# Optimization experiments

Measured on AMD Instinct MI355X. Metric: run time of the kernel, lower is better.

## Reference

```python
import jax, jax.numpy as jnp
import numpy as np

B, IN, C, M = 256, 512, 4, 6
S1, S2 = 255, 63          # neurons per layer excluding the prepended bias unit
K = 2 ** M                # contexts per neuron
P = 1e-3                  # pred_clipping
LMIN = float(np.log(P / (1.0 - P)))
LMAX = -LMIN
LR = 1e-3                 # constant learning rate
WCLIP = 5.0               # weight_clipping
BASE_BIAS = 0.0           # fixed base bias logit (original draws uniform in [LMIN, LMAX])


def setup_inputs() -> dict:
    key = jax.random.key(0)
    ks = jax.random.split(key, 10)
    x = jax.random.uniform(ks[0], (B, IN), dtype=jnp.float32)
    target = jax.random.randint(ks[1], (B,), 0, C, dtype=jnp.int32)
    cmaps1 = jax.random.normal(ks[2], (C, S1, M, IN), dtype=jnp.float32)
    w1 = jax.random.uniform(ks[3], (C, S1, K, IN), dtype=jnp.float32) * (2.0 / IN)
    bias1 = jax.random.uniform(ks[4], (1, 1, C), dtype=jnp.float32, minval=LMIN, maxval=LMAX)
    cmaps2 = jax.random.normal(ks[5], (C, S2, M, IN), dtype=jnp.float32)
    w2 = jax.random.uniform(ks[6], (C, S2, K, S1 + 1), dtype=jnp.float32) * (2.0 / (S1 + 1))
    bias2 = jax.random.uniform(ks[7], (1, 1, C), dtype=jnp.float32, minval=LMIN, maxval=LMAX)
    cmaps3 = jax.random.normal(ks[8], (C, 1, M, IN), dtype=jnp.float32)
    w3 = jax.random.uniform(ks[9], (C, 1, K, S2 + 1), dtype=jnp.float32) * (2.0 / (S2 + 1))
    return {"x": x, "target": target, "cmaps1": cmaps1, "w1": w1, "bias1": bias1,
            "cmaps2": cmaps2, "w2": w2, "bias2": bias2, "cmaps3": cmaps3, "w3": w3}


def _layer(logit3, context, tgt, cmaps, weights, bias):
    # logit3: (B, I, Cin) with Cin in {1, C}; context: (B, IN); tgt: (B, C) one-hot
    # cmaps: (C, S, M, IN); weights: (C, S, K, I)
    Cn, S = weights.shape[0], weights.shape[1]
    Bn = context.shape[0]
    # context halfspace gating -> per-(class, neuron, sample) context index
    dist = jnp.einsum('csmk,bk->csmb', cmaps, context)          # (C,S,M,B)
    conv = (2 ** jnp.arange(M, dtype=jnp.int32)).reshape(1, 1, M, 1)
    idx = jnp.sum((dist > 0.0).astype(jnp.int32) * conv, axis=2)  # (C,S,B)
    ci = jnp.arange(Cn)[:, None, None]
    si = jnp.arange(S)[None, :, None]
    sel = weights[ci, si, idx]                                  # gather: (C,S,B,I)
    lg = jnp.broadcast_to(logit3, (Bn, logit3.shape[1], Cn))    # (B,I,C)
    out = jnp.clip(jnp.einsum('csbi,bic->csb', sel, lg), LMIN, LMAX)
    out_t = jnp.transpose(out, (2, 1, 0))                       # (B,S,C)
    # online gradient-style update scattered back into the weight table
    diff = jax.nn.sigmoid(out_t) - tgt[:, None, :]              # (B,S,C)
    upd = LR * diff[..., None] * jnp.transpose(lg, (0, 2, 1))[:, None, :, :]  # (B,S,C,I)
    new_w = weights.at[ci, si, idx].set(
        jnp.clip(sel - jnp.transpose(upd, (2, 1, 0, 3)), -WCLIP, WCLIP))
    if bias is not None:
        out_t = jnp.concatenate([jnp.broadcast_to(bias, (Bn, 1, Cn)), out_t], axis=1)
    return out_t, new_w


def reference(x, target, cmaps1, w1, bias1, cmaps2, w2, bias2, cmaps3, w3):
    tgt = jax.nn.one_hot(target, C, dtype=x.dtype)              # (B,C)
    xb = jnp.clip(x, P, 1.0 - P)
    l0 = jnp.log(xb / (1.0 - xb)).at[:, 0].set(BASE_BIAS)       # base predictions in logit space
    out1, nw1 = _layer(l0[:, :, None], x, tgt, cmaps1, w1, bias1)  # (B,256,C)
    out2, nw2 = _layer(out1, x, tgt, cmaps2, w2, bias2)            # (B,64,C)
    out3, nw3 = _layer(out2, x, tgt, cmaps3, w3, None)             # (B,1,C)
    logits = out3[:, 0, :]                                         # (B,C)
    return (logits, nw1, nw2, nw3)
```

## Files before the change

kernel.cpp:

```cpp
#include <hip/hip_runtime.h>
#include <math.h>

#define B_   256
#define IN_  512
#define C_   4
#define M_   6
#define K_   64
#define S1_  255
#define S2_  63

#define NBLK1 (C_ * S1_)
#define NBLK2 (C_ * S2_)
#define NBLK3 (C_)
#define NBLK_ALL (NBLK1 + NBLK2 + NBLK3)

#define LMIN_ (-6.906754778648554f)
#define LMAX_ ( 6.906754778648554f)
#define LR_   0.001f
#define WCLIP_ 5.0f

typedef float v4f __attribute__((ext_vector_type(4)));

__device__ __forceinline__ float clampf(float v, float lo, float hi) {
    return fminf(fmaxf(v, lo), hi);
}

__global__ __launch_bounds__(256) void prep_kernel(const float* __restrict__ x,
                                                   const float* __restrict__ bias1,
                                                   const float* __restrict__ bias2,
                                                   float* __restrict__ xT,
                                                   float* __restrict__ l0,
                                                   float* __restrict__ l0T,
                                                   float* __restrict__ out1T,
                                                   float* __restrict__ out1RM,
                                                   float* __restrict__ out2T,
                                                   float* __restrict__ out2RM) {
    __shared__ float tx_[32][33];
    __shared__ float tl_[32][33];
    const int i0 = (blockIdx.x & 15) * 32;
    const int b0 = (blockIdx.x >> 4) * 32;
    const int tx = threadIdx.x & 31;
    const int ty = threadIdx.x >> 5;
#pragma unroll
    for (int r = 0; r < 4; ++r) {
        int bb = b0 + ty + 8 * r;
        int ii = i0 + tx;
        float xv = x[(size_t)bb * IN_ + ii];
        float xc = clampf(xv, 0.001f, 0.999f);
        float lv = (ii == 0) ? 0.0f : logf(xc / (1.0f - xc));
        l0[(size_t)bb * IN_ + ii] = lv;
        tx_[ty + 8 * r][tx] = xv;
        tl_[ty + 8 * r][tx] = lv;
    }
    __syncthreads();
#pragma unroll
    for (int r = 0; r < 4; ++r) {
        int ii = i0 + ty + 8 * r;
        int bb = b0 + tx;
        xT[(size_t)ii * B_ + bb]  = tx_[tx][ty + 8 * r];
        l0T[(size_t)ii * B_ + bb] = tl_[tx][ty + 8 * r];
    }
    int gid = blockIdx.x * 256 + threadIdx.x;
    if (gid < C_ * B_) {
        int c = gid >> 8, b = gid & 255;
        float b1 = bias1[c], b2 = bias2[c];
        out1T[((size_t)c * (S1_ + 1)) * B_ + b] = b1;
        out1RM[((size_t)c * B_ + b) * (S1_ + 1)] = b1;
        out2T[((size_t)c * (S2_ + 1)) * B_ + b] = b2;
        out2RM[((size_t)c * B_ + b) * (S2_ + 1)] = b2;
    }
}

__global__ __launch_bounds__(256) void route_kernel(
    const float* __restrict__ xT,
    const float* __restrict__ cmaps1,
    const float* __restrict__ cmaps2,
    const float* __restrict__ cmaps3,
    int* __restrict__ idx_buf)
{
    __shared__ float sacc[3][2][M_][B_];
    const int wv   = __builtin_amdgcn_readfirstlane(threadIdx.x >> 6);
    const int lane = threadIdx.x & 63;
    const int t0   = blockIdx.x * 2;

    const float* cmp[2];
#pragma unroll
    for (int u = 0; u < 2; ++u) {
        int bid = t0 + u;
        if (bid < NBLK1)              cmp[u] = cmaps1 + (size_t)bid * M_ * IN_;
        else if (bid < NBLK1 + NBLK2) cmp[u] = cmaps2 + (size_t)(bid - NBLK1) * M_ * IN_;
        else                          cmp[u] = cmaps3 + (size_t)(bid - NBLK1 - NBLK2) * M_ * IN_;
    }

    float acc[2][4][M_];
#pragma unroll
    for (int u = 0; u < 2; ++u)
#pragma unroll
        for (int jb = 0; jb < 4; ++jb)
#pragma unroll
            for (int m = 0; m < M_; ++m) acc[u][jb][m] = 0.0f;

    const int kw = wv * 128;
    for (int k0 = kw; k0 < kw + 128; k0 += 8) {
        float xv[8][4];
#pragma unroll
        for (int j = 0; j < 8; ++j)
#pragma unroll
            for (int jb = 0; jb < 4; ++jb)
                xv[j][jb] = xT[(size_t)(k0 + j) * B_ + 64 * jb + lane];
#pragma unroll
        for (int j = 0; j < 8; ++j)
#pragma unroll
            for (int u = 0; u < 2; ++u)
#pragma unroll
                for (int m = 0; m < M_; ++m) {
                    float cv = cmp[u][(size_t)m * IN_ + k0 + j];
#pragma unroll
                    for (int jb = 0; jb < 4; ++jb)
                        acc[u][jb][m] = fmaf(cv, xv[j][jb], acc[u][jb][m]);
                }
    }

    if (wv > 0) {
#pragma unroll
        for (int u = 0; u < 2; ++u)
#pragma unroll
            for (int jb = 0; jb < 4; ++jb)
#pragma unroll
                for (int m = 0; m < M_; ++m)
                    sacc[wv - 1][u][m][64 * jb + lane] = acc[u][jb][m];
    }
    __syncthreads();
    if (wv == 0) {
#pragma unroll
        for (int u = 0; u < 2; ++u)
#pragma unroll
            for (int jb = 0; jb < 4; ++jb) {
                int b = 64 * jb + lane;
                int myidx = 0;
#pragma unroll
                for (int m = 0; m < M_; ++m) {
                    float t = acc[u][jb][m] + sacc[0][u][m][b] + sacc[1][u][m][b] + sacc[2][u][m][b];
                    myidx |= (t > 0.0f) ? (1 << m) : 0;
                }
                idx_buf[(size_t)(t0 + u) * B_ + b] = myidx;
            }
    }
}


template<int DIN, int KSPL>
__device__ __forceinline__ void dot_body(
    int bid,
    const float* __restrict__ lgT, long lgT_sc,
    const float* __restrict__ w,
    const int* __restrict__ idx_buf,
    float* __restrict__ pdot,
    int S, float* wl)
{
    constexpr int KR  = DIN / KSPL;
    static_assert(KR == 64, "k-slice must be 64");
    constexpr int PAD = 65;

    const int tile = bid / KSPL;
    const int ks   = bid % KSPL;
    const int c    = tile / S;
    const int tid  = threadIdx.x;
    const int b    = tid;
    const int k0   = ks * KR;

    const int myrow = idx_buf[(size_t)tile * B_ + b];

    const float* wp = w + (size_t)tile * K_ * DIN + k0;
#pragma unroll
    for (int j = 0; j < 4; ++j) {
        int f   = tid + 256 * j;
        int row = f >> 4;
        int q   = (f & 15) << 2;
        float4 v = *(const float4*)(wp + (size_t)row * DIN + q);
        wl[row * PAD + q + 0] = v.x;
        wl[row * PAD + q + 1] = v.y;
        wl[row * PAD + q + 2] = v.z;
        wl[row * PAD + q + 3] = v.w;
    }
    __syncthreads();

    const float* lgp = lgT + (size_t)c * lgT_sc + (size_t)k0 * B_ + b;
    const float* wr  = wl + myrow * PAD;
    float dot = 0.0f;
    for (int kk = 0; kk < KR; kk += 8) {
        float lv[8];
#pragma unroll
        for (int t = 0; t < 8; ++t) lv[t] = lgp[(size_t)(kk + t) * B_];
#pragma unroll
        for (int t = 0; t < 8; ++t) dot = fmaf(wr[kk + t], lv[t], dot);
    }
    pdot[((size_t)tile * KSPL + ks) * B_ + b] = dot;
}

template<int DIN>
__device__ __forceinline__ void update_body(
    int ub,
    const float* __restrict__ w,
    const float* __restrict__ lgRM, long lg_sc,
    const int* __restrict__ win_g,
    const float* __restrict__ dw_g,
    float* __restrict__ nw,
    int SK)
{
    constexpr int QPR = DIN / 4;
    constexpr int QSH = (DIN == 512) ? 7 : (DIN == 256) ? 6 : 4;
    const int base = ub * 2048 + threadIdx.x;
#pragma unroll
    for (int j = 0; j < 8; ++j) {
        int Q   = base + j * 256;
        int row = Q >> QSH;
        int col = (Q & (QPR - 1)) << 2;
        float4 wv = *(const float4*)(w + (size_t)row * DIN + col);
        int bw = win_g[row];
        if (bw >= 0) {
            float d = dw_g[row];
            int cc  = row / SK;
            const float4 lv = *(const float4*)(lgRM + (size_t)cc * lg_sc + (size_t)bw * DIN + col);
            wv.x = clampf(wv.x - d * lv.x, -WCLIP_, WCLIP_);
            wv.y = clampf(wv.y - d * lv.y, -WCLIP_, WCLIP_);
            wv.z = clampf(wv.z - d * lv.z, -WCLIP_, WCLIP_);
            wv.w = clampf(wv.w - d * lv.w, -WCLIP_, WCLIP_);
        }
        v4f o = {wv.x, wv.y, wv.z, wv.w};
        __builtin_nontemporal_store(o, (v4f*)(nw + (size_t)row * DIN + col));
    }
}

template<int DIN, int KSPL>
__global__ __launch_bounds__(256) void dot_kernel(
    const float* __restrict__ lgT, long lgT_sc,
    const float* __restrict__ w,
    const int* __restrict__ idx_buf,
    float* __restrict__ pdot, int S)
{
    __shared__ float wl[K_ * 65];
    dot_body<DIN, KSPL>(blockIdx.x, lgT, lgT_sc, w, idx_buf, pdot, S, wl);
}

__global__ __launch_bounds__(256) void fin_kernel(
    const float* __restrict__ pdot, int KSPL,
    const int* __restrict__ idx_buf,
    const int* __restrict__ target,
    float* __restrict__ onextT,
    float* __restrict__ onextRM,
    int* __restrict__ win_g,
    float* __restrict__ dw_g,
    int S)
{
    __shared__ float diff_s[B_];
    __shared__ int   win_s[K_];
    const int tile = blockIdx.x;
    const int c    = tile / S;
    const int s    = tile - c * S;
    const int b    = threadIdx.x;

    if (b < K_) win_s[b] = -1;

    float dot = 0.0f;
    for (int j = 0; j < KSPL; ++j)
        dot += pdot[((size_t)tile * KSPL + j) * B_ + b];

    float outv = clampf(dot, LMIN_, LMAX_);
    onextT[((size_t)c * (S + 1) + (s + 1)) * B_ + b] = outv;
    onextRM[((size_t)c * B_ + b) * (size_t)(S + 1) + (s + 1)] = outv;

    float tg = (target[b] == c) ? 1.0f : 0.0f;
    diff_s[b] = 1.0f / (1.0f + expf(-outv)) - tg;
    const int myrow = idx_buf[(size_t)tile * B_ + b];
    __syncthreads();
    atomicMax(&win_s[myrow], b);
    __syncthreads();
    if (b < K_) {
        int bw = win_s[b];
        win_g[(size_t)tile * K_ + b] = bw;
        dw_g[(size_t)tile * K_ + b]  = (bw >= 0) ? LR_ * diff_s[bw] : 0.0f;
    }
}

template<int DIN_D, int KSPL_D, int DIN_U>
__global__ __launch_bounds__(256) void mix_kernel(
    const float* __restrict__ lgT, long lgT_sc,
    const float* __restrict__ wD,
    const int* __restrict__ idxD,
    float* __restrict__ pdot, int SD, int ndot,
    const float* __restrict__ wU,
    const float* __restrict__ lgRM, long lg_sc,
    const int* __restrict__ win_g,
    const float* __restrict__ dw_g,
    float* __restrict__ nwU, int SKU)
{
    __shared__ float wl[K_ * 65];
    if ((int)blockIdx.x < ndot)
        dot_body<DIN_D, KSPL_D>(blockIdx.x, lgT, lgT_sc, wD, idxD, pdot, SD, wl);
    else
        update_body<DIN_U>(blockIdx.x - ndot, wU, lgRM, lg_sc, win_g, dw_g, nwU, SKU);
}

__global__ __launch_bounds__(256) void fin3u_kernel(
    const float* __restrict__ pdot,
    const int* __restrict__ idx3,
    const int* __restrict__ target,
    const float* __restrict__ lgRM, long lg_sc,
    const float* __restrict__ w3,
    float* __restrict__ nw3,
    float* __restrict__ logits)
{
    __shared__ float diff_s[B_];
    __shared__ float dw_s[K_];
    __shared__ int   win_s[K_];
    const int c = blockIdx.x;
    const int b = threadIdx.x;

    if (b < K_) win_s[b] = -1;

    float outv = clampf(pdot[(size_t)c * B_ + b], LMIN_, LMAX_);
    logits[(size_t)b * C_ + c] = outv;
    float tg = (target[b] == c) ? 1.0f : 0.0f;
    diff_s[b] = 1.0f / (1.0f + expf(-outv)) - tg;
    const int myrow = idx3[(size_t)c * B_ + b];
    __syncthreads();
    atomicMax(&win_s[myrow], b);
    __syncthreads();
    if (b < K_) {
        int bw = win_s[b];
        dw_s[b] = (bw >= 0) ? LR_ * diff_s[bw] : 0.0f;
    }
    __syncthreads();

    const float* lgc = lgRM + (size_t)c * lg_sc;
    const float* wp  = w3  + (size_t)c * K_ * 64;
    float*       nwp = nw3 + (size_t)c * K_ * 64;
#pragma unroll
    for (int j = 0; j < 4; ++j) {
        int Q   = b + 256 * j;
        int row = Q >> 4;
        int col = (Q & 15) << 2;
        float4 wv = *(const float4*)(wp + row * 64 + col);
        int bw = win_s[row];
        if (bw >= 0) {
            float d = dw_s[row];
            const float4 lv = *(const float4*)(lgc + (size_t)bw * 64 + col);
            wv.x = clampf(wv.x - d * lv.x, -WCLIP_, WCLIP_);
            wv.y = clampf(wv.y - d * lv.y, -WCLIP_, WCLIP_);
            wv.z = clampf(wv.z - d * lv.z, -WCLIP_, WCLIP_);
            wv.w = clampf(wv.w - d * lv.w, -WCLIP_, WCLIP_);
        }
        v4f o = {wv.x, wv.y, wv.z, wv.w};
        __builtin_nontemporal_store(o, (v4f*)(nwp + row * 64 + col));
    }
}

extern "C" void kernel_launch(void* const* d_in, const int* in_sizes, int n_in,
                              void* d_out, int out_size, void* d_ws, size_t ws_size,
                              hipStream_t stream) {
    const float* x      = (const float*)d_in[0];
    const int*   target = (const int*)  d_in[1];
    const float* cmaps1 = (const float*)d_in[2];
    const float* w1     = (const float*)d_in[3];
    const float* bias1  = (const float*)d_in[4];
    const float* cmaps2 = (const float*)d_in[5];
    const float* w2     = (const float*)d_in[6];
    const float* bias2  = (const float*)d_in[7];
    const float* cmaps3 = (const float*)d_in[8];
    const float* w3     = (const float*)d_in[9];
    float* out = (float*)d_out;

    float* xT      = (float*)d_ws;
    float* l0      = xT     + (size_t)IN_ * B_;
    float* l0T     = l0     + (size_t)B_ * IN_;
    float* out1T   = l0T    + (size_t)IN_ * B_;
    float* out1RM  = out1T  + (size_t)C_ * (S1_ + 1) * B_;
    float* out2T   = out1RM + (size_t)C_ * B_ * (S1_ + 1);
    float* out2RM  = out2T  + (size_t)C_ * (S2_ + 1) * B_;
    float* pdot    = out2RM + (size_t)C_ * B_ * (S2_ + 1);
    float* dw_g    = pdot   + (size_t)NBLK1 * 8 * B_;
    int*   win_g   = (int*)(dw_g + (size_t)NBLK_ALL * K_);
    int*   idx_buf = (int*)(win_g + (size_t)NBLK_ALL * K_);

    float* logits = out;
    float* nw1 = out + (size_t)B_ * C_;
    float* nw2 = nw1 + (size_t)C_ * S1_ * K_ * IN_;
    float* nw3 = nw2 + (size_t)C_ * S2_ * K_ * (S1_ + 1);

    const int* idx1 = idx_buf;
    const int* idx2 = idx_buf + (size_t)NBLK1 * B_;
    const int* idx3 = idx_buf + (size_t)(NBLK1 + NBLK2) * B_;
    int*   win1 = win_g;                         float* dw1 = dw_g;
    int*   win2 = win_g + NBLK1 * K_;            float* dw2 = dw_g + NBLK1 * K_;

    prep_kernel<<<dim3(128), dim3(256), 0, stream>>>(
        x, bias1, bias2, xT, l0, l0T, out1T, out1RM, out2T, out2RM);

    route_kernel<<<dim3(NBLK_ALL / 2), dim3(256), 0, stream>>>(
        xT, cmaps1, cmaps2, cmaps3, idx_buf);

    dot_kernel<512, 8><<<dim3(NBLK1 * 8), dim3(256), 0, stream>>>(
        l0T, 0L, w1, idx1, pdot, S1_);
    fin_kernel<<<dim3(NBLK1), dim3(256), 0, stream>>>(
        pdot, 8, idx1, target, out1T, out1RM, win1, dw1, S1_);

    mix_kernel<256, 4, 512><<<dim3(NBLK2 * 4 + NBLK1 * 4), dim3(256), 0, stream>>>(
        out1T, (long)(S1_ + 1) * B_, w2, idx2, pdot, S2_, NBLK2 * 4,
        w1, l0, 0L, win1, dw1, nw1, S1_ * K_);
    fin_kernel<<<dim3(NBLK2), dim3(256), 0, stream>>>(
        pdot, 4, idx2, target, out2T, out2RM, win2, dw2, S2_);

    mix_kernel<64, 1, 256><<<dim3(NBLK3 + NBLK2 * 2), dim3(256), 0, stream>>>(
        out2T, (long)(S2_ + 1) * B_, w3, idx3, pdot, 1, NBLK3,
        w2, out1RM, (long)B_ * (S1_ + 1), win2, dw2, nw2, S2_ * K_);

    fin3u_kernel<<<dim3(NBLK3), dim3(256), 0, stream>>>(
        pdot, idx3, target, out2RM, (long)B_ * (S2_ + 1), w3, nw3, logits);
}
```

Before: 138.2 us.

## Fuse dot and finalize stages into 512-thread blocks, removing pdot round-trips

Split-K dot kernels and their separate finalize kernels are merged: each tile is now handled by one 512-thread block whose two halves each cover half of the input dimension and reduce through shared memory before doing clamp, sigmoid diff and winner selection in place. This removes the pdot global buffer, two kernel launches and the serialization between partial-dot and finalize passes. The last-layer update reuses the weights staged in LDS instead of reloading them. The trade-off is fewer, larger blocks for layer 1 (1020 instead of 8160), which lowers parallelism and gives less latency hiding while each block walks over K sequentially.

```diff
diff --git a/kernel.cpp b/kernel.cpp
--- a/kernel.cpp
+++ b/kernel.cpp
@@ -148,54 +148,77 @@
     }
 }
 
-
-template<int DIN, int KSPL>
-__device__ __forceinline__ void dot_body(
-    int bid,
+template<int DIN>
+__device__ __forceinline__ void dotfin_body(
+    int tile,
     const float* __restrict__ lgT, long lgT_sc,
     const float* __restrict__ w,
     const int* __restrict__ idx_buf,
-    float* __restrict__ pdot,
-    int S, float* wl)
-{
-    constexpr int KR  = DIN / KSPL;
-    static_assert(KR == 64, "k-slice must be 64");
-    constexpr int PAD = 65;
-
-    const int tile = bid / KSPL;
-    const int ks   = bid % KSPL;
-    const int c    = tile / S;
-    const int tid  = threadIdx.x;
-    const int b    = tid;
-    const int k0   = ks * KR;
-
+    const int* __restrict__ target,
+    float* __restrict__ onextT,
+    float* __restrict__ onextRM,
+    int* __restrict__ win_g,
+    float* __restrict__ dw_g,
+    int S,
+    float* wl, float* part_s, float* diff_s, int* win_s)
+{
+    constexpr int HALF = DIN / 2;
+    constexpr int NR   = HALF / 64;
+    const int c   = tile / S;
+    const int s   = tile - c * S;
+    const int tid = threadIdx.x;
+    const int kh  = __builtin_amdgcn_readfirstlane(tid >> 8);
+    const int b   = tid & 255;
+
+    if (tid < K_) win_s[tid] = -1;
     const int myrow = idx_buf[(size_t)tile * B_ + b];
 
-    const float* wp = w + (size_t)tile * K_ * DIN + k0;
-#pragma unroll
-    for (int j = 0; j < 4; ++j) {
-        int f   = tid + 256 * j;
-        int row = f >> 4;
-        int q   = (f & 15) << 2;
-        float4 v = *(const float4*)(wp + (size_t)row * DIN + q);
-        wl[row * PAD + q + 0] = v.x;
-        wl[row * PAD + q + 1] = v.y;
-        wl[row * PAD + q + 2] = v.z;
-        wl[row * PAD + q + 3] = v.w;
-    }
-    __syncthreads();
-
-    const float* lgp = lgT + (size_t)c * lgT_sc + (size_t)k0 * B_ + b;
-    const float* wr  = wl + myrow * PAD;
+    const float* wp  = w + (size_t)tile * K_ * DIN + kh * HALF;
+    float*       dst = wl + kh * (K_ * 65);
     float dot = 0.0f;
-    for (int kk = 0; kk < KR; kk += 8) {
-        float lv[8];
-#pragma unroll
-        for (int t = 0; t < 8; ++t) lv[t] = lgp[(size_t)(kk + t) * B_];
-#pragma unroll
-        for (int t = 0; t < 8; ++t) dot = fmaf(wr[kk + t], lv[t], dot);
-    }
-    pdot[((size_t)tile * KSPL + ks) * B_ + b] = dot;
+#pragma unroll
+    for (int r = 0; r < NR; ++r) {
+        const float* src = wp + r * 64;
+#pragma unroll
+        for (int j = 0; j < 4; ++j) {
+            int f   = b + 256 * j;
+            int row = f >> 4;
+            int q   = (f & 15) << 2;
+            float4 v = *(const float4*)(src + (size_t)row * DIN + q);
+            dst[row * 65 + q + 0] = v.x;
+            dst[row * 65 + q + 1] = v.y;
+            dst[row * 65 + q + 2] = v.z;
+            dst[row * 65 + q + 3] = v.w;
+        }
+        __syncthreads();
+        const float* lgp = lgT + (size_t)c * lgT_sc + (size_t)(kh * HALF + r * 64) * B_ + b;
+        const float* wr  = dst + myrow * 65;
+        for (int kk = 0; kk < 64; kk += 8) {
+            float lv[8];
+#pragma unroll
+            for (int t = 0; t < 8; ++t) lv[t] = lgp[(size_t)(kk + t) * B_];
+#pragma unroll
+            for (int t = 0; t < 8; ++t) dot = fmaf(wr[kk + t], lv[t], dot);
+        }
+        __syncthreads();
+    }
+    if (kh == 1) part_s[b] = dot;
+    __syncthreads();
+    if (kh == 0) {
+        float total = dot + part_s[b];
+        float outv = clampf(total, LMIN_, LMAX_);
+        onextT[((size_t)c * (S + 1) + (s + 1)) * B_ + b] = outv;
+        onextRM[((size_t)c * B_ + b) * (size_t)(S + 1) + (s + 1)] = outv;
+        float tg = (target[b] == c) ? 1.0f : 0.0f;
+        diff_s[b] = 1.0f / (1.0f + expf(-outv)) - tg;
+        atomicMax(&win_s[myrow], b);
+    }
+    __syncthreads();
+    if (tid < K_) {
+        int bw = win_s[tid];
+        win_g[(size_t)tile * K_ + tid] = bw;
+        dw_g[(size_t)tile * K_ + tid]  = (bw >= 0) ? LR_ * diff_s[bw] : 0.0f;
+    }
 }
 
 template<int DIN>
@@ -209,11 +232,11 @@
     int SK)
 {
     constexpr int QPR = DIN / 4;
-    constexpr int QSH = (DIN == 512) ? 7 : (DIN == 256) ? 6 : 4;
+    constexpr int QSH = (DIN == 512) ? 7 : 6;
     const int base = ub * 2048 + threadIdx.x;
 #pragma unroll
-    for (int j = 0; j < 8; ++j) {
-        int Q   = base + j * 256;
+    for (int j = 0; j < 4; ++j) {
+        int Q   = base + j * 512;
         int row = Q >> QSH;
         int col = (Q & (QPR - 1)) << 2;
         float4 wv = *(const float4*)(w + (size_t)row * DIN + col);
@@ -232,116 +255,109 @@
     }
 }
 
-template<int DIN, int KSPL>
-__global__ __launch_bounds__(256) void dot_kernel(
-    const float* __restrict__ lgT, long lgT_sc,
-    const float* __restrict__ w,
-    const int* __restrict__ idx_buf,
-    float* __restrict__ pdot, int S)
-{
-    __shared__ float wl[K_ * 65];
-    dot_body<DIN, KSPL>(blockIdx.x, lgT, lgT_sc, w, idx_buf, pdot, S, wl);
-}
-
-__global__ __launch_bounds__(256) void fin_kernel(
-    const float* __restrict__ pdot, int KSPL,
-    const int* __restrict__ idx_buf,
+__global__ __launch_bounds__(512) void dotfin1_kernel(
+    const float* __restrict__ l0T,
+    const float* __restrict__ w1,
+    const int* __restrict__ idx1,
     const int* __restrict__ target,
-    float* __restrict__ onextT,
-    float* __restrict__ onextRM,
-    int* __restrict__ win_g,
-    float* __restrict__ dw_g,
-    int S)
-{
+    float* __restrict__ out1T, float* __restrict__ out1RM,
+    int* __restrict__ win1, float* __restrict__ dw1)
+{
+    __shared__ float wl[2 * K_ * 65];
+    __shared__ float part_s[B_];
     __shared__ float diff_s[B_];
     __shared__ int   win_s[K_];
-    const int tile = blockIdx.x;
-    const int c    = tile / S;
-    const int s    = tile - c * S;
-    const int b    = threadIdx.x;
-
-    if (b < K_) win_s[b] = -1;
-
-    float dot = 0.0f;
-    for (int j = 0; j < KSPL; ++j)
-        dot += pdot[((size_t)tile * KSPL + j) * B_ + b];
-
-    float outv = clampf(dot, LMIN_, LMAX_);
-    onextT[((size_t)c * (S + 1) + (s + 1)) * B_ + b] = outv;
-    onextRM[((size_t)c * B_ + b) * (size_t)(S + 1) + (s + 1)] = outv;
-
-    float tg = (target[b] == c) ? 1.0f : 0.0f;
-    diff_s[b] = 1.0f / (1.0f + expf(-outv)) - tg;
-    const int myrow = idx_buf[(size_t)tile * B_ + b];
-    __syncthreads();
-    atomicMax(&win_s[myrow], b);
-    __syncthreads();
-    if (b < K_) {
-        int bw = win_s[b];
-        win_g[(size_t)tile * K_ + b] = bw;
-        dw_g[(size_t)tile * K_ + b]  = (bw >= 0) ? LR_ * diff_s[bw] : 0.0f;
-    }
-}
-
-template<int DIN_D, int KSPL_D, int DIN_U>
-__global__ __launch_bounds__(256) void mix_kernel(
+    dotfin_body<512>(blockIdx.x, l0T, 0L, w1, idx1, target,
+                     out1T, out1RM, win1, dw1, S1_, wl, part_s, diff_s, win_s);
+}
+
+__global__ __launch_bounds__(512) void mix2_kernel(
+    const float* __restrict__ out1T,
+    const float* __restrict__ w2,
+    const int* __restrict__ idx2,
+    const int* __restrict__ target,
+    float* __restrict__ out2T, float* __restrict__ out2RM,
+    int* __restrict__ win2, float* __restrict__ dw2,
+    const float* __restrict__ w1,
+    const float* __restrict__ l0,
+    const int* __restrict__ win1, const float* __restrict__ dw1,
+    float* __restrict__ nw1, int ndot)
+{
+    __shared__ float wl[2 * K_ * 65];
+    __shared__ float part_s[B_];
+    __shared__ float diff_s[B_];
+    __shared__ int   win_s[K_];
+    if ((int)blockIdx.x < ndot)
+        dotfin_body<256>(blockIdx.x, out1T, (long)(S1_ + 1) * B_, w2, idx2, target,
+                         out2T, out2RM, win2, dw2, S2_, wl, part_s, diff_s, win_s);
+    else
+        update_body<512>(blockIdx.x - ndot, w1, l0, 0L, win1, dw1, nw1, S1_ * K_);
+}
+
+__device__ __forceinline__ void dotfinup3_body(
+    int c,
     const float* __restrict__ lgT, long lgT_sc,
-    const float* __restrict__ wD,
-    const int* __restrict__ idxD,
-    float* __restrict__ pdot, int SD, int ndot,
-    const float* __restrict__ wU,
     const float* __restrict__ lgRM, long lg_sc,
-    const int* __restrict__ win_g,
-    const float* __restrict__ dw_g,
-    float* __restrict__ nwU, int SKU)
-{
-    __shared__ float wl[K_ * 65];
-    if ((int)blockIdx.x < ndot)
-        dot_body<DIN_D, KSPL_D>(blockIdx.x, lgT, lgT_sc, wD, idxD, pdot, SD, wl);
-    else
-        update_body<DIN_U>(blockIdx.x - ndot, wU, lgRM, lg_sc, win_g, dw_g, nwU, SKU);
-}
-
-__global__ __launch_bounds__(256) void fin3u_kernel(
-    const float* __restrict__ pdot,
+    const float* __restrict__ w3,
     const int* __restrict__ idx3,
     const int* __restrict__ target,
-    const float* __restrict__ lgRM, long lg_sc,
-    const float* __restrict__ w3,
     float* __restrict__ nw3,
-    float* __restrict__ logits)
-{
-    __shared__ float diff_s[B_];
-    __shared__ float dw_s[K_];
-    __shared__ int   win_s[K_];
-    const int c = blockIdx.x;
-    const int b = threadIdx.x;
-
-    if (b < K_) win_s[b] = -1;
-
-    float outv = clampf(pdot[(size_t)c * B_ + b], LMIN_, LMAX_);
-    logits[(size_t)b * C_ + c] = outv;
-    float tg = (target[b] == c) ? 1.0f : 0.0f;
-    diff_s[b] = 1.0f / (1.0f + expf(-outv)) - tg;
+    float* __restrict__ logits,
+    float* wl , float* part_s, float* diff_s, float* dw_s, int* win_s)
+{
+    const int tid = threadIdx.x;
+    const int kh  = __builtin_amdgcn_readfirstlane(tid >> 8);
+    const int b   = tid & 255;
+    if (tid < K_) win_s[tid] = -1;
     const int myrow = idx3[(size_t)c * B_ + b];
-    __syncthreads();
-    atomicMax(&win_s[myrow], b);
-    __syncthreads();
-    if (b < K_) {
-        int bw = win_s[b];
-        dw_s[b] = (bw >= 0) ? LR_ * diff_s[bw] : 0.0f;
-    }
+
+    const float* wp  = w3 + (size_t)c * K_ * 64 + kh * 32;
+    float*       dst = wl + kh * (K_ * 33);
+#pragma unroll
+    for (int j = 0; j < 2; ++j) {
+        int f   = b + 256 * j;
+        int row = f >> 3;
+        int q   = (f & 7) << 2;
+        float4 v = *(const float4*)(wp + (size_t)row * 64 + q);
+        dst[row * 33 + q + 0] = v.x;
+        dst[row * 33 + q + 1] = v.y;
+        dst[row * 33 + q + 2] = v.z;
+        dst[row * 33 + q + 3] = v.w;
+    }
+    __syncthreads();
+    const float* lgp = lgT + (size_t)c * lgT_sc + (size_t)(kh * 32) * B_ + b;
+    const float* wr  = dst + myrow * 33;
+    float dot = 0.0f;
+    for (int kk = 0; kk < 32; kk += 8) {
+        float lv[8];
+#pragma unroll
+        for (int t = 0; t < 8; ++t) lv[t] = lgp[(size_t)(kk + t) * B_];
+#pragma unroll
+        for (int t = 0; t < 8; ++t) dot = fmaf(wr[kk + t], lv[t], dot);
+    }
+    if (kh == 1) part_s[b] = dot;
+    __syncthreads();
+    if (kh == 0) {
+        float total = dot + part_s[b];
+        float outv = clampf(total, LMIN_, LMAX_);
+        logits[(size_t)b * C_ + c] = outv;
+        float tg = (target[b] == c) ? 1.0f : 0.0f;
+        diff_s[b] = 1.0f / (1.0f + expf(-outv)) - tg;
+        atomicMax(&win_s[myrow], b);
+    }
+    __syncthreads();
+    if (tid < K_) dw_s[tid] = (win_s[tid] >= 0) ? LR_ * diff_s[win_s[tid]] : 0.0f;
     __syncthreads();
 
     const float* lgc = lgRM + (size_t)c * lg_sc;
-    const float* wp  = w3  + (size_t)c * K_ * 64;
-    float*       nwp = nw3 + (size_t)c * K_ * 64;
-#pragma unroll
-    for (int j = 0; j < 4; ++j) {
-        int Q   = b + 256 * j;
+    float* nwp = nw3 + (size_t)c * K_ * 64;
+#pragma unroll
+    for (int j = 0; j < 2; ++j) {
+        int Q   = tid + 512 * j;
         int row = Q >> 4;
         int col = (Q & 15) << 2;
-        float4 wv = *(const float4*)(wp + row * 64 + col);
+        const float* wsrc = wl + (col >> 5) * (K_ * 33) + row * 33 + (col & 31);
+        float4 wv = {wsrc[0], wsrc[1], wsrc[2], wsrc[3]};
         int bw = win_s[row];
         if (bw >= 0) {
             float d = dw_s[row];
@@ -352,8 +368,35 @@
             wv.w = clampf(wv.w - d * lv.w, -WCLIP_, WCLIP_);
         }
         v4f o = {wv.x, wv.y, wv.z, wv.w};
-        __builtin_nontemporal_store(o, (v4f*)(nwp + row * 64 + col));
-    }
+        __builtin_nontemporal_store(o, (v4f*)(nwp + (size_t)row * 64 + col));
+    }
+}
+
+__global__ __launch_bounds__(512) void mix3_kernel(
+    const float* __restrict__ out2T,
+    const float* __restrict__ out2RM,
+    const float* __restrict__ w3,
+    const int* __restrict__ idx3,
+    const int* __restrict__ target,
+    float* __restrict__ nw3,
+    float* __restrict__ logits,
+    const float* __restrict__ w2,
+    const float* __restrict__ out1RM,
+    const int* __restrict__ win2, const float* __restrict__ dw2,
+    float* __restrict__ nw2, int ndot)
+{
+    __shared__ float wl[2 * K_ * 33];
+    __shared__ float part_s[B_];
+    __shared__ float diff_s[B_];
+    __shared__ float dw_s[K_];
+    __shared__ int   win_s[K_];
+    if ((int)blockIdx.x < ndot)
+        dotfinup3_body(blockIdx.x, out2T, (long)(S2_ + 1) * B_,
+                       out2RM, (long)B_ * (S2_ + 1), w3, idx3, target,
+                       nw3, logits, wl, part_s, diff_s, dw_s, win_s);
+    else
+        update_body<256>(blockIdx.x - ndot, w2, out1RM, (long)B_ * (S1_ + 1),
+                         win2, dw2, nw2, S2_ * K_);
 }
 
 extern "C" void kernel_launch(void* const* d_in, const int* in_sizes, int n_in,
@@ -378,8 +421,7 @@
     float* out1RM  = out1T  + (size_t)C_ * (S1_ + 1) * B_;
     float* out2T   = out1RM + (size_t)C_ * B_ * (S1_ + 1);
     float* out2RM  = out2T  + (size_t)C_ * (S2_ + 1) * B_;
-    float* pdot    = out2RM + (size_t)C_ * B_ * (S2_ + 1);
-    float* dw_g    = pdot   + (size_t)NBLK1 * 8 * B_;
+    float* dw_g    = out2RM + (size_t)C_ * B_ * (S2_ + 1);
     int*   win_g   = (int*)(dw_g + (size_t)NBLK_ALL * K_);
     int*   idx_buf = (int*)(win_g + (size_t)NBLK_ALL * K_);
 
@@ -391,8 +433,8 @@
     const int* idx1 = idx_buf;
     const int* idx2 = idx_buf + (size_t)NBLK1 * B_;
     const int* idx3 = idx_buf + (size_t)(NBLK1 + NBLK2) * B_;
-    int*   win1 = win_g;                         float* dw1 = dw_g;
-    int*   win2 = win_g + NBLK1 * K_;            float* dw2 = dw_g + NBLK1 * K_;
+    int*   win1 = win_g;                float* dw1 = dw_g;
+    int*   win2 = win_g + NBLK1 * K_;   float* dw2 = dw_g + NBLK1 * K_;
 
     prep_kernel<<<dim3(128), dim3(256), 0, stream>>>(
         x, bias1, bias2, xT, l0, l0T, out1T, out1RM, out2T, out2RM);
@@ -400,21 +442,14 @@
     route_kernel<<<dim3(NBLK_ALL / 2), dim3(256), 0, stream>>>(
         xT, cmaps1, cmaps2, cmaps3, idx_buf);
 
-    dot_kernel<512, 8><<<dim3(NBLK1 * 8), dim3(256), 0, stream>>>(
-        l0T, 0L, w1, idx1, pdot, S1_);
-    fin_kernel<<<dim3(NBLK1), dim3(256), 0, stream>>>(
-        pdot, 8, idx1, target, out1T, out1RM, win1, dw1, S1_);
-
-    mix_kernel<256, 4, 512><<<dim3(NBLK2 * 4 + NBLK1 * 4), dim3(256), 0, stream>>>(
-        out1T, (long)(S1_ + 1) * B_, w2, idx2, pdot, S2_, NBLK2 * 4,
-        w1, l0, 0L, win1, dw1, nw1, S1_ * K_);
-    fin_kernel<<<dim3(NBLK2), dim3(256), 0, stream>>>(
-        pdot, 4, idx2, target, out2T, out2RM, win2, dw2, S2_);
-
-    mix_kernel<64, 1, 256><<<dim3(NBLK3 + NBLK2 * 2), dim3(256), 0, stream>>>(
-        out2T, (long)(S2_ + 1) * B_, w3, idx3, pdot, 1, NBLK3,
-        w2, out1RM, (long)B_ * (S1_ + 1), win2, dw2, nw2, S2_ * K_);
-
-    fin3u_kernel<<<dim3(NBLK3), dim3(256), 0, stream>>>(
-        pdot, idx3, target, out2RM, (long)B_ * (S2_ + 1), w3, nw3, logits);
-}
+    dotfin1_kernel<<<dim3(NBLK1), dim3(512), 0, stream>>>(
+        l0T, w1, idx1, target, out1T, out1RM, win1, dw1);
+
+    mix2_kernel<<<dim3(NBLK2 + NBLK1 * 4), dim3(512), 0, stream>>>(
+        out1T, w2, idx2, target, out2T, out2RM, win2, dw2,
+        w1, l0, win1, dw1, nw1, NBLK2);
+
+    mix3_kernel<<<dim3(NBLK3 + NBLK2 * 64 * 64 / 2048), dim3(512), 0, stream>>>(
+        out2T, out2RM, w3, idx3, target, nw3, logits,
+        w2, out1RM, win2, dw2, nw2, NBLK3);
+}
```

Result: faster. 126.6 us (-8.4%).
